# Optimization experiments

Hardware: AMD Instinct MI355X
Metric: run time of the kernel (lower is better)

The kernel has to match this reference:

```python
import jax, jax.numpy as jnp
import numpy as np

B, D, C = 512, 512, 85742   # batch, in_features, out_features (MS1M identities)
M = 4                       # angular margin order -> cos(4*theta) = 8c^4 - 8c^2 + 1
PI = 3.14159265             # constant used in the torch source
LAMB = max(5.0, 1000.0 * (1.0 + 0.12 * 1) ** -1.0)  # lamb at iter=1 (first forward)
EPS = 1e-12                 # torch F.normalize eps


def setup_inputs() -> dict:
    key = jax.random.key(0)
    k1, k2, k3 = jax.random.split(key, 3)
    x = jax.random.normal(k1, (B, D), dtype=jnp.float32)
    label = jax.random.randint(k2, (B,), 0, C)
    limit = np.sqrt(6.0 / (D + C))  # xavier_uniform bound for weight [C, D]
    weight = jax.random.uniform(k3, (C, D), minval=-limit, maxval=limit, dtype=jnp.float32)
    return {"x": x, "weight": weight, "label": label}


def reference(x, weight, label):
    # row-normalize features and class weights (F.normalize, p=2, dim=1)
    xn = x / jnp.maximum(jnp.linalg.norm(x, axis=1, keepdims=True), EPS)
    wn = weight / jnp.maximum(jnp.linalg.norm(weight, axis=1, keepdims=True), EPS)
    cos = jnp.clip(xn @ wn.T, -1.0, 1.0)                       # [B, C] cosine logits
    cos_m = 8.0 * cos**4 - 8.0 * cos**2 + 1.0                  # cos(4*theta), m=4
    # theta/k computed on detached cos (torch uses cos_theta.data)
    theta = jnp.arccos(jax.lax.stop_gradient(cos))
    k = jnp.floor(M * theta / PI)
    phi = (-1.0) ** k * cos_m - 2.0 * k                        # [B, C]
    feat_norm = jnp.linalg.norm(x, axis=1)                     # [B]
    one_hot = jax.nn.one_hot(label, C, dtype=cos.dtype)        # scatter of 1s at label
    out = (one_hot * (phi - cos) / (1.0 + LAMB) + cos) * feat_norm[:, None]
    # cross-entropy, mean reduction
    logp = jax.nn.log_softmax(out, axis=1)
    loss = -jnp.take_along_axis(logp, label[:, None], axis=1).mean()
    return loss
```

## Files before the change

### kernel.cpp

```cpp
#include <hip/hip_runtime.h>
#include <stdint.h>

#define D_K 512
#define C_CLS 85742
#define N_TILES 670
#define N_PART (N_TILES * 2)

using bf16x8 = __attribute__((ext_vector_type(8))) short;
using f32x4  = __attribute__((ext_vector_type(4))) float;

__device__ __forceinline__ unsigned int cvtpk(float a, float b) {
  unsigned int r;
  asm("v_cvt_pk_bf16_f32 %0, %1, %2" : "=v"(r) : "v"(a), "v"(b));
  return r;
}
__device__ __forceinline__ unsigned short f2bf(float f) {
  unsigned int u = __builtin_bit_cast(unsigned int, f);
  u += 0x7FFFu + ((u >> 16) & 1u);
  return (unsigned short)(u >> 16);
}
__device__ __forceinline__ float bf2f(unsigned short h) {
  return __builtin_bit_cast(float, ((unsigned int)h) << 16);
}
__device__ __forceinline__ float sq8(const float4& a, const float4& b) {
  return a.x*a.x + a.y*a.y + a.z*a.z + a.w*a.w +
         b.x*b.x + b.y*b.y + b.z*b.z + b.w*b.w;
}

__global__ __launch_bounds__(256) void k_xnorm(const float* __restrict__ X,
                                               unsigned short* __restrict__ XN,
                                               float* __restrict__ FN) {
  int row  = blockIdx.x * 4 + (threadIdx.x >> 6);
  int lane = threadIdx.x & 63;
  const float4* px = (const float4*)(X + (size_t)row * D_K + lane * 8);
  float4 u = px[0], v = px[1];
  float nsq = sq8(u, v);
#pragma unroll
  for (int m = 1; m <= 32; m <<= 1) nsq += __shfl_xor(nsq, m);
  float nrm = sqrtf(nsq);
  float inv = 1.0f / fmaxf(nrm, 1e-12f);
  uint4 o;
  o.x = cvtpk(u.x*inv, u.y*inv); o.y = cvtpk(u.z*inv, u.w*inv);
  o.z = cvtpk(v.x*inv, v.y*inv); o.w = cvtpk(v.z*inv, v.w*inv);
  *(uint4*)(XN + (size_t)row * D_K + lane * 8) = o;
  if (lane == 0) FN[row] = nrm;
}

__global__ __launch_bounds__(512) void k_gemm_lse(const float* __restrict__ W,
                                                  const unsigned short* __restrict__ XN,
                                                  const float* __restrict__ FN,
                                                  float2* __restrict__ PART) {
  __shared__ alignas(16) unsigned short As[2][4096];
  __shared__ alignas(16) unsigned short Bs[2][4096];
  __shared__ float nsqS[128];
  __shared__ float fnS[128];

  int bid = blockIdx.x;
  int wg    = (bid & 7) * 335 + (bid >> 3);
  int ntile = wg >> 2, mtile = wg & 3;
  int m0 = mtile * 128, n0 = ntile * 128;

  int t    = threadIdx.x;
  int lane = t & 63, wid = t >> 6;
  int wm = wid >> 1, wn = wid & 1;
  int s = lane & 15, g = lane >> 4;

  int rB = t >> 2;
  int gr = n0 + rB; if (gr > C_CLS - 1) gr = C_CLS - 1;
  const float* pB = W + (size_t)gr * D_K + (t & 3) * 8;

  const unsigned short* gA0 = XN + (size_t)(m0 + wid * 16 + (lane >> 2)) * D_K + (lane & 3) * 8;

  f32x4 acc[2][4] = {};
  float nsq = 0.f;
  float4 xa0, xa1;
  float4 ya0, ya1;

#define GLDS(srcp, dstp) __builtin_amdgcn_global_load_lds( \
    (const __attribute__((address_space(1))) unsigned int*)(srcp), \
    (__attribute__((address_space(3))) unsigned int*)(dstp), 16, 0, 0)

#define STAGE_A(b, kk) GLDS(gA0 + (size_t)(kk) * 32, &As[b][wid * 512])

#define PREF_X(kk) do { const float* q_ = pB + (size_t)(kk) * 32; \
    xa0 = *(const float4*)q_; xa1 = *(const float4*)(q_ + 4); } while (0)
#define PREF_Y(kk) do { const float* q_ = pB + (size_t)(kk) * 32; \
    ya0 = *(const float4*)q_; ya1 = *(const float4*)(q_ + 4); } while (0)

#define CONV_X(b) do { nsq += sq8(xa0, xa1); \
    uint4 u_; u_.x = cvtpk(xa0.x, xa0.y); u_.y = cvtpk(xa0.z, xa0.w); \
    u_.z = cvtpk(xa1.x, xa1.y); u_.w = cvtpk(xa1.z, xa1.w); \
    *(uint4*)(&Bs[b][rB * 32 + (t & 3) * 8]) = u_; } while (0)
#define CONV_Y(b) do { nsq += sq8(ya0, ya1); \
    uint4 u_; u_.x = cvtpk(ya0.x, ya0.y); u_.y = cvtpk(ya0.z, ya0.w); \
    u_.z = cvtpk(ya1.x, ya1.y); u_.w = cvtpk(ya1.z, ya1.w); \
    *(uint4*)(&Bs[b][rB * 32 + (t & 3) * 8]) = u_; } while (0)

#define FRAGS_MFMA(b) do { \
    bf16x8 af[2], bfr[4]; \
    _Pragma("unroll") for (int mf = 0; mf < 2; ++mf) \
      af[mf] = *(const bf16x8*)(&As[b][(wm * 32 + mf * 16 + s) * 32 + g * 8]); \
    _Pragma("unroll") for (int nf = 0; nf < 4; ++nf) \
      bfr[nf] = *(const bf16x8*)(&Bs[b][(wn * 64 + nf * 16 + s) * 32 + g * 8]); \
    _Pragma("unroll") for (int mf = 0; mf < 2; ++mf) \
      _Pragma("unroll") for (int nf = 0; nf < 4; ++nf) \
        acc[mf][nf] = __builtin_amdgcn_mfma_f32_16x16x32_bf16(af[mf], bfr[nf], acc[mf][nf], 0, 0, 0); \
  } while (0)

#define BARC() do { \
    asm volatile("s_waitcnt vmcnt(2) lgkmcnt(0)" ::: "memory"); \
    __builtin_amdgcn_s_barrier(); } while (0)
#define BAR0() do { \
    asm volatile("s_waitcnt vmcnt(0) lgkmcnt(0)" ::: "memory"); \
    __builtin_amdgcn_s_barrier(); } while (0)

  STAGE_A(0, 0);
  PREF_X(0);
  PREF_Y(1);
  if (t < 128) fnS[t] = FN[m0 + t];
  CONV_X(0);
  BARC();

  for (int kt = 0; kt < 14; kt += 2) {
    STAGE_A(1, kt + 1);
    PREF_X(kt + 2);
    FRAGS_MFMA(0);
    CONV_Y(1);
    BARC();
    STAGE_A(0, kt + 2);
    PREF_Y(kt + 3);
    FRAGS_MFMA(1);
    CONV_X(0);
    BARC();
  }
  STAGE_A(1, 15);
  FRAGS_MFMA(0);
  CONV_Y(1);
  BAR0();
  FRAGS_MFMA(1);

  nsq += __shfl_xor(nsq, 1); nsq += __shfl_xor(nsq, 2);
  if ((t & 3) == 0) nsqS[rB] = nsq;
  __syncthreads();

  float rinv[4]; int cvalid[4];
#pragma unroll
  for (int nf = 0; nf < 4; ++nf) {
    int cl = wn * 64 + nf * 16 + s;
    cvalid[nf] = (n0 + cl) < C_CLS;
    rinv[nf] = 1.0f / fmaxf(sqrtf(nsqS[cl]), 1e-12f);
  }
  const float NEG_INF = -__builtin_inff();
#pragma unroll
  for (int mf = 0; mf < 2; ++mf) {
#pragma unroll
    for (int q = 0; q < 4; ++q) {
      int rl = wm * 32 + mf * 16 + g * 4 + q;
      float fr = fnS[rl];
      float z[4]; float mx = NEG_INF;
#pragma unroll
      for (int nf = 0; nf < 4; ++nf) {
        float cc = acc[mf][nf][q] * rinv[nf];
        cc = fminf(fmaxf(cc, -1.0f), 1.0f);
        z[nf] = cvalid[nf] ? cc * fr : NEG_INF;
        mx = fmaxf(mx, z[nf]);
      }
#pragma unroll
      for (int d = 1; d <= 8; d <<= 1) mx = fmaxf(mx, __shfl_xor(mx, d));
      float se = 0.f;
#pragma unroll
      for (int nf = 0; nf < 4; ++nf) se += __expf(z[nf] - mx);
#pragma unroll
      for (int d = 1; d <= 8; d <<= 1) se += __shfl_xor(se, d);
      if (s == mf * 4 + q)
        PART[(size_t)(m0 + rl) * N_PART + (ntile * 2 + wn)] = make_float2(mx, se);
    }
  }
}

__global__ __launch_bounds__(64) void k_target(const float* __restrict__ W,
                                               const unsigned short* __restrict__ XN,
                                               const float* __restrict__ FN,
                                               const int* __restrict__ LBL,
                                               float2* __restrict__ ZT) {
  int row = blockIdx.x;
  int lane = threadIdx.x;
  int lab = LBL[row];
  const float* pw = W + (size_t)lab * D_K + lane * 8;
  const unsigned short* px = XN + (size_t)row * D_K + lane * 8;
  float dot = 0.f, nsq = 0.f;
#pragma unroll
  for (int j = 0; j < 8; ++j) {
    float w = pw[j];
    nsq += w * w;
    dot += bf2f(px[j]) * bf2f(f2bf(w));
  }
#pragma unroll
  for (int m = 1; m <= 32; m <<= 1) { dot += __shfl_xor(dot, m); nsq += __shfl_xor(nsq, m); }
  if (lane == 0) {
    const float LAMB = 1000.0f / 1.12f;
    float rinv = 1.0f / fmaxf(sqrtf(nsq), 1e-12f);
    float c = fminf(fmaxf(dot * rinv, -1.0f), 1.0f);
    float c2 = c * c;
    float cm = 8.0f * c2 * c2 - 8.0f * c2 + 1.0f;
    float th = acosf(c);
    float kf = floorf(4.0f * th / 3.14159265f);
    float phi = ((((int)kf) & 1) ? -cm : cm) - 2.0f * kf;
    float fr = FN[row];
    float zu = fr * c;
    float zm = fr * (c + (phi - c) / (1.0f + LAMB));
    ZT[row] = make_float2(zu, zm);
  }
}

__global__ __launch_bounds__(256) void k_lse(const float2* __restrict__ PART,
                                             const float2* __restrict__ ZT,
                                             float* __restrict__ LOSSI) {
  int row = blockIdx.x;
  int t = threadIdx.x;
  const float NEG_INF = -__builtin_inff();
  float m = NEG_INF, ss = 0.f;
  for (int p = t; p < N_PART; p += 256) {
    float2 ps = PART[(size_t)row * N_PART + p];
    if (ps.y > 0.f) {
      if (ps.x > m) { ss = ss * __expf(m - ps.x) + ps.y; m = ps.x; }
      else          { ss += ps.y * __expf(ps.x - m); }
    }
  }
  __shared__ float sm[256], sv[256];
  sm[t] = m; sv[t] = ss;
  __syncthreads();
  for (int o = 128; o > 0; o >>= 1) {
    if (t < o) {
      float m1 = sm[t], s1 = sv[t];
      float m2 = sm[t + o], s2 = sv[t + o];
      float mm = fmaxf(m1, m2);
      float e1 = (m1 > NEG_INF) ? s1 * __expf(m1 - mm) : 0.f;
      float e2 = (m2 > NEG_INF) ? s2 * __expf(m2 - mm) : 0.f;
      sm[t] = mm; sv[t] = e1 + e2;
    }
    __syncthreads();
  }
  if (t == 0) {
    float M = sm[0], S = sv[0];
    float2 zt = ZT[row];
    S += __expf(zt.y - M) - __expf(zt.x - M);
    LOSSI[row] = M + logf(S) - zt.y;
  }
}

__global__ __launch_bounds__(256) void k_mean(const float* __restrict__ LOSSI,
                                              float* __restrict__ OUT) {
  int t = threadIdx.x;
  float s_ = LOSSI[t] + LOSSI[t + 256];
#pragma unroll
  for (int m = 1; m <= 32; m <<= 1) s_ += __shfl_xor(s_, m);
  __shared__ float wsum[4];
  if ((t & 63) == 0) wsum[t >> 6] = s_;
  __syncthreads();
  if (t == 0) OUT[0] = (wsum[0] + wsum[1] + wsum[2] + wsum[3]) * (1.0f / 512.0f);
}

extern "C" void kernel_launch(void* const* d_in, const int* in_sizes, int n_in,
                              void* d_out, int out_size, void* d_ws, size_t ws_size,
                              hipStream_t stream) {
  const float* X   = (const float*)d_in[0];
  const float* W   = (const float*)d_in[1];
  const int*   LBL = (const int*)d_in[2];
  float* OUT = (float*)d_out;

  char* ws = (char*)d_ws;
  unsigned short* XN = (unsigned short*)ws;
  float*  FN    = (float*)(ws + 524288);
  float2* ZT    = (float2*)(ws + 526336);
  float*  LOSSI = (float*)(ws + 530432);
  float2* PART  = (float2*)(ws + 532480);

  k_xnorm  <<<dim3(128),  dim3(256), 0, stream>>>(X, XN, FN);
  k_gemm_lse<<<dim3(2680), dim3(512), 0, stream>>>(W, XN, FN, PART);
  k_target <<<dim3(512),  dim3(64),  0, stream>>>(W, XN, FN, LBL, ZT);
  k_lse    <<<dim3(512),  dim3(256), 0, stream>>>(PART, ZT, LOSSI);
  k_mean   <<<dim3(1),    dim3(256), 0, stream>>>(LOSSI, OUT);
}
```

Baseline: 109.0 us.

## Retile GEMM so each block covers all 512 rows for a 64-class strip

The GEMM+LSE kernel is retiled so that each 1024-thread block computes the full 512-row batch against a 64-class strip of W. Before, 128x128 tiles made four blocks each read and convert the same W rows. Now every W row is read from global memory and converted to bf16 exactly once. The A (XN) tile staged in LDS grows to cover the whole batch and gets an XOR swizzle, and B rows are padded to 40 elements to avoid bank conflicts. In exchange, the block is much larger and uses more LDS, which may limit occupancy. Each thread also issues narrower per-thread W loads (float2).

```diff
diff --git a/kernel.cpp b/kernel.cpp
--- a/kernel.cpp
+++ b/kernel.cpp
@@ -3,8 +3,7 @@
 
 #define D_K 512
 #define C_CLS 85742
-#define N_TILES 670
-#define N_PART (N_TILES * 2)
+#define N_PART 1340
 
 using bf16x8 = __attribute__((ext_vector_type(8))) short;
 using f32x4  = __attribute__((ext_vector_type(4))) float;
@@ -26,6 +25,10 @@
   return a.x*a.x + a.y*a.y + a.z*a.z + a.w*a.w +
          b.x*b.x + b.y*b.y + b.z*b.z + b.w*b.w;
 }
+
+#define GLDS(srcp, dstp) __builtin_amdgcn_global_load_lds( \
+    (const __attribute__((address_space(1))) unsigned int*)(srcp), \
+    (__attribute__((address_space(3))) unsigned int*)(dstp), 16, 0, 0)
 
 __global__ __launch_bounds__(256) void k_xnorm(const float* __restrict__ X,
                                                unsigned short* __restrict__ XN,
@@ -46,117 +49,108 @@
   if (lane == 0) FN[row] = nrm;
 }
 
-__global__ __launch_bounds__(512) void k_gemm_lse(const float* __restrict__ W,
-                                                  const unsigned short* __restrict__ XN,
-                                                  const float* __restrict__ FN,
-                                                  float2* __restrict__ PART) {
-  __shared__ alignas(16) unsigned short As[2][4096];
-  __shared__ alignas(16) unsigned short Bs[2][4096];
-  __shared__ float nsqS[128];
-  __shared__ float fnS[128];
+__global__ __launch_bounds__(1024, 4) void k_gemm_lse(const float* __restrict__ W,
+                                                      const unsigned short* __restrict__ XN,
+                                                      const float* __restrict__ FN,
+                                                      float2* __restrict__ PART) {
+  __shared__ alignas(16) unsigned short As[2][16384];
+  __shared__ alignas(16) unsigned short Bs[2][2560];
+  __shared__ float nsqS[64];
 
   int bid = blockIdx.x;
-  int wg    = (bid & 7) * 335 + (bid >> 3);
-  int ntile = wg >> 2, mtile = wg & 3;
-  int m0 = mtile * 128, n0 = ntile * 128;
+  int n0 = bid * 64;
 
   int t    = threadIdx.x;
   int lane = t & 63, wid = t >> 6;
-  int wm = wid >> 1, wn = wid & 1;
   int s = lane & 15, g = lane >> 4;
 
-  int rB = t >> 2;
-  int gr = n0 + rB; if (gr > C_CLS - 1) gr = C_CLS - 1;
-  const float* pB = W + (size_t)gr * D_K + (t & 3) * 8;
-
-  const unsigned short* gA0 = XN + (size_t)(m0 + wid * 16 + (lane >> 2)) * D_K + (lane & 3) * 8;
+  int rA = (lane >> 2);
+  int lcA = (lane & 3) ^ ((lane >> 3) & 3);
+  const unsigned short* gA0 = XN + (size_t)((wid * 2 + 0) * 16 + rA) * D_K + lcA * 8;
+  const unsigned short* gA1 = XN + (size_t)((wid * 2 + 1) * 16 + rA) * D_K + lcA * 8;
+
+  int rB = t >> 4, cB = t & 15;
+  int grB = n0 + rB; if (grB > C_CLS - 1) grB = C_CLS - 1;
+  const float* pB = W + (size_t)grB * D_K + cB * 2;
 
   f32x4 acc[2][4] = {};
   float nsq = 0.f;
-  float4 xa0, xa1;
-  float4 ya0, ya1;
-
-#define GLDS(srcp, dstp) __builtin_amdgcn_global_load_lds( \
-    (const __attribute__((address_space(1))) unsigned int*)(srcp), \
-    (__attribute__((address_space(3))) unsigned int*)(dstp), 16, 0, 0)
-
-#define STAGE_A(b, kk) GLDS(gA0 + (size_t)(kk) * 32, &As[b][wid * 512])
-
-#define PREF_X(kk) do { const float* q_ = pB + (size_t)(kk) * 32; \
-    xa0 = *(const float4*)q_; xa1 = *(const float4*)(q_ + 4); } while (0)
-#define PREF_Y(kk) do { const float* q_ = pB + (size_t)(kk) * 32; \
-    ya0 = *(const float4*)q_; ya1 = *(const float4*)(q_ + 4); } while (0)
-
-#define CONV_X(b) do { nsq += sq8(xa0, xa1); \
-    uint4 u_; u_.x = cvtpk(xa0.x, xa0.y); u_.y = cvtpk(xa0.z, xa0.w); \
-    u_.z = cvtpk(xa1.x, xa1.y); u_.w = cvtpk(xa1.z, xa1.w); \
-    *(uint4*)(&Bs[b][rB * 32 + (t & 3) * 8]) = u_; } while (0)
-#define CONV_Y(b) do { nsq += sq8(ya0, ya1); \
-    uint4 u_; u_.x = cvtpk(ya0.x, ya0.y); u_.y = cvtpk(ya0.z, ya0.w); \
-    u_.z = cvtpk(ya1.x, ya1.y); u_.w = cvtpk(ya1.z, ya1.w); \
-    *(uint4*)(&Bs[b][rB * 32 + (t & 3) * 8]) = u_; } while (0)
+  float2 bx, by;
+
+#define STAGE_A(b, kk) do { \
+    GLDS(gA0 + (size_t)(kk) * 32, &As[b][(wid * 2 + 0) * 512]); \
+    GLDS(gA1 + (size_t)(kk) * 32, &As[b][(wid * 2 + 1) * 512]); \
+  } while (0)
+
+#define LDB(kk) (*(const float2*)(pB + (size_t)(kk) * 32))
+
+#define CVTW(bv, b) do { \
+    nsq += bv.x * bv.x + bv.y * bv.y; \
+    *(unsigned int*)(&Bs[b][rB * 40 + cB * 2]) = cvtpk(bv.x, bv.y); \
+  } while (0)
 
 #define FRAGS_MFMA(b) do { \
     bf16x8 af[2], bfr[4]; \
-    _Pragma("unroll") for (int mf = 0; mf < 2; ++mf) \
-      af[mf] = *(const bf16x8*)(&As[b][(wm * 32 + mf * 16 + s) * 32 + g * 8]); \
+    _Pragma("unroll") for (int mf = 0; mf < 2; ++mf) { \
+      int R_ = wid * 32 + mf * 16 + s; \
+      af[mf] = *(const bf16x8*)(&As[b][R_ * 32 + (g ^ ((s >> 1) & 3)) * 8]); \
+    } \
     _Pragma("unroll") for (int nf = 0; nf < 4; ++nf) \
-      bfr[nf] = *(const bf16x8*)(&Bs[b][(wn * 64 + nf * 16 + s) * 32 + g * 8]); \
+      bfr[nf] = *(const bf16x8*)(&Bs[b][(nf * 16 + s) * 40 + g * 8]); \
     _Pragma("unroll") for (int mf = 0; mf < 2; ++mf) \
       _Pragma("unroll") for (int nf = 0; nf < 4; ++nf) \
         acc[mf][nf] = __builtin_amdgcn_mfma_f32_16x16x32_bf16(af[mf], bfr[nf], acc[mf][nf], 0, 0, 0); \
   } while (0)
 
-#define BARC() do { \
-    asm volatile("s_waitcnt vmcnt(2) lgkmcnt(0)" ::: "memory"); \
+#define BARC1() do { \
+    asm volatile("s_waitcnt vmcnt(1) lgkmcnt(0)" ::: "memory"); \
     __builtin_amdgcn_s_barrier(); } while (0)
 #define BAR0() do { \
     asm volatile("s_waitcnt vmcnt(0) lgkmcnt(0)" ::: "memory"); \
     __builtin_amdgcn_s_barrier(); } while (0)
 
   STAGE_A(0, 0);
-  PREF_X(0);
-  PREF_Y(1);
-  if (t < 128) fnS[t] = FN[m0 + t];
-  CONV_X(0);
-  BARC();
+  bx = LDB(0);
+  by = LDB(1);
+  CVTW(bx, 0);
+  BARC1();
 
   for (int kt = 0; kt < 14; kt += 2) {
     STAGE_A(1, kt + 1);
-    PREF_X(kt + 2);
+    bx = LDB(kt + 2);
     FRAGS_MFMA(0);
-    CONV_Y(1);
-    BARC();
+    CVTW(by, 1);
+    BARC1();
     STAGE_A(0, kt + 2);
-    PREF_Y(kt + 3);
+    by = LDB(kt + 3);
     FRAGS_MFMA(1);
-    CONV_X(0);
-    BARC();
+    CVTW(bx, 0);
+    BARC1();
   }
   STAGE_A(1, 15);
   FRAGS_MFMA(0);
-  CONV_Y(1);
+  CVTW(by, 1);
   BAR0();
   FRAGS_MFMA(1);
 
   nsq += __shfl_xor(nsq, 1); nsq += __shfl_xor(nsq, 2);
-  if ((t & 3) == 0) nsqS[rB] = nsq;
+  nsq += __shfl_xor(nsq, 4); nsq += __shfl_xor(nsq, 8);
+  if ((lane & 15) == 0) nsqS[rB] = nsq;
   __syncthreads();
 
   float rinv[4]; int cvalid[4];
 #pragma unroll
   for (int nf = 0; nf < 4; ++nf) {
-    int cl = wn * 64 + nf * 16 + s;
-    cvalid[nf] = (n0 + cl) < C_CLS;
-    rinv[nf] = 1.0f / fmaxf(sqrtf(nsqS[cl]), 1e-12f);
+    cvalid[nf] = (n0 + nf * 16 + s) < C_CLS;
+    rinv[nf] = 1.0f / fmaxf(sqrtf(nsqS[nf * 16 + s]), 1e-12f);
   }
   const float NEG_INF = -__builtin_inff();
 #pragma unroll
   for (int mf = 0; mf < 2; ++mf) {
 #pragma unroll
     for (int q = 0; q < 4; ++q) {
-      int rl = wm * 32 + mf * 16 + g * 4 + q;
-      float fr = fnS[rl];
+      int rl = wid * 32 + mf * 16 + g * 4 + q;
+      float fr = FN[rl];
       float z[4]; float mx = NEG_INF;
 #pragma unroll
       for (int nf = 0; nf < 4; ++nf) {
@@ -173,7 +167,7 @@
 #pragma unroll
       for (int d = 1; d <= 8; d <<= 1) se += __shfl_xor(se, d);
       if (s == mf * 4 + q)
-        PART[(size_t)(m0 + rl) * N_PART + (ntile * 2 + wn)] = make_float2(mx, se);
+        PART[(size_t)rl * N_PART + bid] = make_float2(mx, se);
     }
   }
 }
@@ -276,9 +270,9 @@
   float*  LOSSI = (float*)(ws + 530432);
   float2* PART  = (float2*)(ws + 532480);
 
-  k_xnorm  <<<dim3(128),  dim3(256), 0, stream>>>(X, XN, FN);
-  k_gemm_lse<<<dim3(2680), dim3(512), 0, stream>>>(W, XN, FN, PART);
-  k_target <<<dim3(512),  dim3(64),  0, stream>>>(W, XN, FN, LBL, ZT);
-  k_lse    <<<dim3(512),  dim3(256), 0, stream>>>(PART, ZT, LOSSI);
-  k_mean   <<<dim3(1),    dim3(256), 0, stream>>>(LOSSI, OUT);
-}
+  k_xnorm  <<<dim3(128),  dim3(256),  0, stream>>>(X, XN, FN);
+  k_gemm_lse<<<dim3(1340), dim3(1024), 0, stream>>>(W, XN, FN, PART);
+  k_target <<<dim3(512),  dim3(64),   0, stream>>>(W, XN, FN, LBL, ZT);
+  k_lse    <<<dim3(512),  dim3(256),  0, stream>>>(PART, ZT, LOSSI);
+  k_mean   <<<dim3(1),    dim3(256),  0, stream>>>(LOSSI, OUT);
+}
```

Result: slower. 140.7 us (+29.1%).
